# Performance work log

Measured on AMD Instinct MI355X. Metric: run time of the kernel, lower is better.

The kernel has to match this reference:

```python
import jax, jax.numpy as jnp
import numpy as np


def setup_inputs() -> dict:
    key = jax.random.key(0)
    k1, k2, k3 = jax.random.split(key, 3)
    N, C, V, T, K = 32, 64, 25, 1024, 3
    x = jax.random.normal(k1, (N, C, V, T), dtype=jnp.float32)
    # grouped 1x1 conv weight: per node v, maps C -> K*C. torch weight (C*K*V, C, 1, 1)
    W = jax.random.normal(k2, (V, K * C, C), dtype=jnp.float32) * 0.05
    # adjacency buffer A[k, w, v] (src node w -> dst node v, partition k)
    A = jax.random.uniform(k3, (K, V, V), dtype=jnp.float32)
    return {"x": x, "W": W, "A": A}


def reference(x, W, A):
    # x: [N, C, V, T]; W: [V, K*C, C]; A: [K, V, V]
    N, C, V, T = x.shape
    K = A.shape[0]
    # permute(0,2,1,3): [N, V, C, T]; grouped 1x1 conv == per-node matmul C -> K*C
    y = jnp.einsum('ncvt,voc->nvot', x, W)          # [N, V, K*C, T]
    # view (N, V, C*K, T) with output-channel layout o = c*K + k -> split to (C, K)
    y = y.reshape(N, V, C, K, T)                     # [N, V(src=w), C, K, T]
    # einsum('kwv,nckwt->ncvt')
    out = jnp.einsum('kwv,nwckt->ncvt', A, y)        # [N, C, V, T]
    return out
```

## Files before the change

kernel.cpp:

```cpp
#include <hip/hip_runtime.h>

#define Nn 32
#define Cc 64
#define Vv 25
#define Tt 1024

typedef __attribute__((ext_vector_type(4))) float f32x4;
typedef __attribute__((ext_vector_type(8))) short bf16x8;
typedef __attribute__((ext_vector_type(4))) unsigned short u16x4;

__device__ __forceinline__ unsigned short f2bf(float f) {
    union { float f; unsigned u; } a; a.f = f;
    unsigned u = a.u;
    u += 0x7fff + ((u >> 16) & 1);
    return (unsigned short)(u >> 16);
}

__device__ __forceinline__ void gl_lds16(const unsigned short* g, unsigned short* l) {
    __builtin_amdgcn_global_load_lds(
        (const __attribute__((address_space(1))) unsigned int*)g,
        (__attribute__((address_space(3))) unsigned int*)l, 16, 0, 0);
}


__global__ __launch_bounds__(256) void prep_fused(
        const float* __restrict__ x, const float* __restrict__ W,
        const float* __restrict__ A, unsigned short* __restrict__ xb,
        unsigned short* __restrict__ Weff) {
    int bid = blockIdx.x;
    if (bid < Vv * Vv) {
        int v = bid / Vv;
        int w = bid - v * Vv;
        float a0 = A[(0 * Vv + w) * Vv + v];
        float a1 = A[(1 * Vv + w) * Vv + v];
        float a2 = A[(2 * Vv + w) * Vv + v];
        const float* Wb = W + (size_t)w * 192 * 64;
        unsigned short* o = Weff + (size_t)(v * Vv + w) * 4096;
        int c  = threadIdx.x >> 2;
        int c0 = (threadIdx.x & 3) * 16;
        #pragma unroll
        for (int i = 0; i < 16; ++i) {
            int cp = c0 + i;
            float val = a0 * Wb[(c * 3 + 0) * 64 + cp]
                      + a1 * Wb[(c * 3 + 1) * 64 + cp]
                      + a2 * Wb[(c * 3 + 2) * 64 + cp];
            int jl = cp >> 3;
            o[c * 64 + ((jl ^ (c & 7)) << 3) + (cp & 7)] = f2bf(val);
        }
        return;
    }
    int pid = bid - Vv * Vv;
    int n = pid / (Vv * 4);
    int rem = pid - n * (Vv * 4);
    int w = rem >> 2;
    int sl = rem & 3;

    int tid = threadIdx.x;
    int wq = tid >> 6;
    int l  = tid & 63;
    int quad = l >> 4, m = l & 15;

    const float* xw = x + ((size_t)n * Cc * Vv + w) * Tt + sl * 256 + wq * 64 + m;
    unsigned short* dst = xb +
        ((((size_t)(n * Vv + w) * 4 + sl) * 2048) + (size_t)wq * 512 + l) * 8;

    #pragma unroll
    for (int kc = 0; kc < 2; ++kc) {
        float vals[4][8];
        #pragma unroll
        for (int kk = 0; kk < 8; ++kk) {
            int cp = (kc * 4 + quad) * 8 + kk;
            const float* row = xw + (size_t)cp * (Vv * Tt);
            #pragma unroll
            for (int ni = 0; ni < 4; ++ni)
                vals[ni][kk] = __builtin_nontemporal_load(row + ni * 16);
        }
        #pragma unroll
        for (int ni = 0; ni < 4; ++ni) {
            bf16x8 o;
            #pragma unroll
            for (int kk = 0; kk < 8; ++kk) o[kk] = (short)f2bf(vals[ni][kk]);
            *(bf16x8*)&dst[(size_t)(kc * 256 + ni * 64) * 8] = o;
        }
    }
}

__global__ __launch_bounds__(256, 2) void gc_fast(
        const unsigned short* __restrict__ xb,
        const unsigned short* __restrict__ Weff,
        float* __restrict__ out) {
    __shared__ __align__(16) unsigned short wa[4][4096];

    int bid = blockIdx.x;
    int xcd = bid & 7;
    int lid = bid >> 3;
    int v = lid % Vv;
    int s = lid / Vv;
    int slice = (xcd << 4) + s;
    int n  = slice >> 2;
    int sl = slice & 3;
    int t0 = sl << 8;

    int tid = threadIdx.x;
    int lane = tid & 63, wv = tid >> 6;
    int m = lane & 15, quad = lane >> 4;

    const unsigned short* wg = Weff + (size_t)v * (Vv * 4096);
    const unsigned short* xbase = xb + ((size_t)(n * Vv * 4 + sl)) * 2048 * 8;

    int coff0 = ((quad)     ^ (m & 7)) << 3;
    int coff1 = ((4 + quad) ^ (m & 7)) << 3;
    int arow[4];
    #pragma unroll
    for (int mi = 0; mi < 4; ++mi) arow[mi] = (mi * 16 + m) * 64;
    int boff[8];
    #pragma unroll
    for (int q = 0; q < 8; ++q) boff[q] = ((wv * 8 + q) * 64 + lane) * 8;

    f32x4 acc[4][4];
    #pragma unroll
    for (int i = 0; i < 4; ++i)
        #pragma unroll
        for (int j = 0; j < 4; ++j)
            acc[i][j] = (f32x4){0.f, 0.f, 0.f, 0.f};

    bf16x8 b0v[8], b1v[8], b2v[8];
    bf16x8 afA[8], afB[8];

#define SB __builtin_amdgcn_sched_barrier(0)
#define VMCNT(N_) asm volatile("s_waitcnt vmcnt(" #N_ ")" ::: "memory")

#define ISSUE_A(WBUF, w_) do { \
    const unsigned short* s_ = wg + (size_t)(w_) * 4096 + tid * 8; \
    gl_lds16(s_,        &wa[WBUF][tid * 8]); \
    gl_lds16(s_ + 2048, &wa[WBUF][2048 + tid * 8]); \
} while (0)

#define ISSUE_B(BN, w_) do { \
    const unsigned short* xw_ = xbase + (size_t)(w_) * 65536; \
    _Pragma("unroll") \
    for (int q_ = 0; q_ < 8; ++q_) \
        BN[q_] = *(const bf16x8*)(xw_ + boff[q_]); \
} while (0)

#define LDREAD(AF, RBUF) do { \
    const unsigned short* cur_ = &wa[RBUF][0]; \
    _Pragma("unroll") \
    for (int mi_ = 0; mi_ < 4; ++mi_) { \
        AF[mi_]     = *(const bf16x8*)(cur_ + arow[mi_] + coff0); \
        AF[mi_ + 4] = *(const bf16x8*)(cur_ + arow[mi_] + coff1); \
    } \
} while (0)

#define COMP(AF, BC) do { \
    __builtin_amdgcn_s_setprio(1); \
    _Pragma("unroll") \
    for (int mi_ = 0; mi_ < 4; ++mi_) \
        _Pragma("unroll") \
        for (int ni_ = 0; ni_ < 4; ++ni_) \
            acc[mi_][ni_] = __builtin_amdgcn_mfma_f32_16x16x32_bf16( \
                AF[mi_], BC[ni_], acc[mi_][ni_], 0, 0, 0); \
    _Pragma("unroll") \
    for (int mi_ = 0; mi_ < 4; ++mi_) \
        _Pragma("unroll") \
        for (int ni_ = 0; ni_ < 4; ++ni_) \
            acc[mi_][ni_] = __builtin_amdgcn_mfma_f32_16x16x32_bf16( \
                AF[mi_ + 4], BC[ni_ + 4], acc[mi_][ni_], 0, 0, 0); \
    __builtin_amdgcn_s_setprio(0); \
} while (0)

#define STEP(AFc, AFn, WB, RB, BC, BN, w_) do { \
    ISSUE_A(WB, (w_) + 2); \
    ISSUE_B(BN, (w_) + 2); \
    SB; VMCNT(18); SB; \
    __builtin_amdgcn_s_barrier(); \
    SB; \
    COMP(AFc, BC); \
    LDREAD(AFn, RB); \
    SB; \
} while (0)

    ISSUE_A(0, 0);
    ISSUE_A(1, 1);
    ISSUE_B(b0v, 0);
    ISSUE_B(b1v, 1);
    SB; VMCNT(16); SB;
    __builtin_amdgcn_s_barrier();
    SB;
    LDREAD(afA, 0);
    SB;

    STEP(afA, afB, 2, 1, b0v, b2v,  0);
    STEP(afB, afA, 3, 2, b1v, b0v,  1);
    STEP(afA, afB, 0, 3, b2v, b1v,  2);
    STEP(afB, afA, 1, 0, b0v, b2v,  3);
    STEP(afA, afB, 2, 1, b1v, b0v,  4);
    STEP(afB, afA, 3, 2, b2v, b1v,  5);
    STEP(afA, afB, 0, 3, b0v, b2v,  6);
    STEP(afB, afA, 1, 0, b1v, b0v,  7);
    STEP(afA, afB, 2, 1, b2v, b1v,  8);
    STEP(afB, afA, 3, 2, b0v, b2v,  9);
    STEP(afA, afB, 0, 3, b1v, b0v, 10);
    STEP(afB, afA, 1, 0, b2v, b1v, 11);
    STEP(afA, afB, 2, 1, b0v, b2v, 12);
    STEP(afB, afA, 3, 2, b1v, b0v, 13);
    STEP(afA, afB, 0, 3, b2v, b1v, 14);
    STEP(afB, afA, 1, 0, b0v, b2v, 15);
    STEP(afA, afB, 2, 1, b1v, b0v, 16);
    STEP(afB, afA, 3, 2, b2v, b1v, 17);
    STEP(afA, afB, 0, 3, b0v, b2v, 18);
    STEP(afB, afA, 1, 0, b1v, b0v, 19);
    STEP(afA, afB, 2, 1, b2v, b1v, 20);
    STEP(afB, afA, 3, 2, b0v, b2v, 21);
    STEP(afA, afB, 0, 3, b1v, b0v, 22);
    SB; VMCNT(8); SB;
    __builtin_amdgcn_s_barrier();
    SB;
    COMP(afB, b2v);
    LDREAD(afA, 0);
    SB;
    VMCNT(0);
    SB;
    COMP(afA, b0v);

#undef STEP
#undef COMP
#undef LDREAD
#undef ISSUE_B
#undef ISSUE_A
#undef VMCNT
#undef SB

    float* og = out + ((size_t)n * Cc * Vv + v) * Tt + t0 + wv * 64 + m;
    #pragma unroll
    for (int mi = 0; mi < 4; ++mi)
        #pragma unroll
        for (int r = 0; r < 4; ++r) {
            int c = mi * 16 + quad * 4 + r;
            float* orow = og + (size_t)c * Vv * Tt;
            #pragma unroll
            for (int ni = 0; ni < 4; ++ni)
                __builtin_nontemporal_store(acc[mi][ni][r], &orow[ni * 16]);
        }
}


__global__ __launch_bounds__(256) void weff_prep_plain(
        const float* __restrict__ W, const float* __restrict__ A,
        unsigned short* __restrict__ Weff) {
    int v = blockIdx.x / Vv;
    int w = blockIdx.x - v * Vv;
    float a0 = A[(0 * Vv + w) * Vv + v];
    float a1 = A[(1 * Vv + w) * Vv + v];
    float a2 = A[(2 * Vv + w) * Vv + v];
    const float* Wb = W + (size_t)w * 192 * 64;
    unsigned short* o = Weff + (size_t)(v * Vv + w) * 4096;
    int e0 = threadIdx.x * 16;
    #pragma unroll
    for (int i = 0; i < 16; ++i) {
        int e = e0 + i;
        int c = e >> 6, cp = e & 63;
        float val = a0 * Wb[(c * 3 + 0) * 64 + cp]
                  + a1 * Wb[(c * 3 + 1) * 64 + cp]
                  + a2 * Wb[(c * 3 + 2) * 64 + cp];
        o[e] = f2bf(val);
    }
}

__global__ __launch_bounds__(256, 2) void gc_plain(
        const float* __restrict__ x, const unsigned short* __restrict__ Weff,
        float* __restrict__ out) {
    __shared__ __align__(16) unsigned short xs[256 * 72];
    __shared__ __align__(16) unsigned short wa[64 * 72];
    int bid = blockIdx.x;
    int xcd = bid & 7;
    int lid = bid >> 3;
    int v, s;
    if (lid < 13 * 16) { v = lid % 13;            s = lid / 13; }
    else { int l2 = lid - 13 * 16; v = 13 + l2 % 12; s = l2 / 12; }
    int slice = (xcd << 4) + s;
    int n  = slice >> 2;
    int t0 = (slice & 3) << 8;
    int tid  = threadIdx.x;
    int lane = tid & 63;
    int wv   = tid >> 6;
    int m    = lane & 15;
    int quad = lane >> 4;
    int cc = tid & 7;
    int tt = tid >> 3;
    f32x4 acc[4][4];
    #pragma unroll
    for (int i = 0; i < 4; ++i)
        #pragma unroll
        for (int j = 0; j < 4; ++j)
            acc[i][j] = (f32x4){0.f, 0.f, 0.f, 0.f};
    const float* xg = x + (size_t)n * Cc * Vv * Tt + t0 + tt * 4;
    const bf16x8* wg = (const bf16x8*)(Weff + (size_t)v * Vv * 4096);
    for (int w = 0; w < Vv; ++w) {
        if (w) __syncthreads();
        #pragma unroll
        for (int r = 0; r < 2; ++r) {
            int q = r * 256 + tid;
            int c = q >> 3, b = q & 7;
            *(bf16x8*)&wa[c * 72 + b * 8] = wg[w * 512 + q];
        }
        {
            bf16x8 rows[8];
            #pragma unroll
            for (int i = 0; i < 8; ++i) {
                int cp = cc * 8 + i;
                const float* p = xg + ((size_t)cp * Vv + w) * Tt;
                float4 f0 = *(const float4*)p;
                float4 f1 = *(const float4*)(p + 128);
                rows[0][i] = (short)f2bf(f0.x); rows[1][i] = (short)f2bf(f0.y);
                rows[2][i] = (short)f2bf(f0.z); rows[3][i] = (short)f2bf(f0.w);
                rows[4][i] = (short)f2bf(f1.x); rows[5][i] = (short)f2bf(f1.y);
                rows[6][i] = (short)f2bf(f1.z); rows[7][i] = (short)f2bf(f1.w);
            }
            #pragma unroll
            for (int j = 0; j < 4; ++j) {
                *(bf16x8*)&xs[(tt * 4 + j) * 72 + cc * 8]       = rows[j];
                *(bf16x8*)&xs[(128 + tt * 4 + j) * 72 + cc * 8] = rows[4 + j];
            }
        }
        __syncthreads();
        #pragma unroll
        for (int kc = 0; kc < 2; ++kc) {
            int ko = kc * 32 + quad * 8;
            bf16x8 afr[4], bfr[4];
            #pragma unroll
            for (int mi = 0; mi < 4; ++mi)
                afr[mi] = *(const bf16x8*)&wa[(mi * 16 + m) * 72 + ko];
            #pragma unroll
            for (int ni = 0; ni < 4; ++ni)
                bfr[ni] = *(const bf16x8*)&xs[(wv * 64 + ni * 16 + m) * 72 + ko];
            #pragma unroll
            for (int mi = 0; mi < 4; ++mi)
                #pragma unroll
                for (int ni = 0; ni < 4; ++ni)
                    acc[mi][ni] = __builtin_amdgcn_mfma_f32_16x16x32_bf16(
                        afr[mi], bfr[ni], acc[mi][ni], 0, 0, 0);
        }
    }
    float* og = out + ((size_t)n * Cc * Vv + v) * Tt + t0 + wv * 64 + m;
    #pragma unroll
    for (int mi = 0; mi < 4; ++mi)
        #pragma unroll
        for (int r = 0; r < 4; ++r) {
            int c = mi * 16 + quad * 4 + r;
            float* orow = og + (size_t)c * Vv * Tt;
            #pragma unroll
            for (int ni = 0; ni < 4; ++ni)
                orow[ni * 16] = acc[mi][ni][r];
        }
}

extern "C" void kernel_launch(void* const* d_in, const int* in_sizes, int n_in,
                              void* d_out, int out_size, void* d_ws, size_t ws_size,
                              hipStream_t stream) {
    const float* x = (const float*)d_in[0];
    const float* W = (const float*)d_in[1];
    const float* A = (const float*)d_in[2];
    float* out = (float*)d_out;

    const size_t xb_elems   = (size_t)Nn * Vv * Tt * 64;
    const size_t weff_elems = (size_t)Vv * Vv * 4096;
    const size_t need = (xb_elems + weff_elems) * sizeof(unsigned short);

    if (ws_size >= need) {
        unsigned short* xb   = (unsigned short*)d_ws;
        unsigned short* Weff = xb + xb_elems;
        prep_fused<<<dim3(Vv * Vv + Nn * Vv * 4), dim3(256), 0, stream>>>(x, W, A, xb, Weff);
        gc_fast<<<dim3(3200), dim3(256), 0, stream>>>(xb, Weff, out);
    } else {
        unsigned short* Weff = (unsigned short*)d_ws;
        weff_prep_plain<<<dim3(Vv * Vv), dim3(256), 0, stream>>>(W, A, Weff);
        gc_plain<<<dim3(3200), dim3(256), 0, stream>>>(x, Weff, out);
    }
}
```

Baseline: 492.3 us.

## Load effective weights directly into registers in MFMA fragment layout, drop LDS staging

The prep kernel now writes Weff pre-arranged in the per-lane MFMA A-fragment order, replacing the XOR-swizzled row layout. The main kernel then loads A fragments straight from global memory into registers, removing the LDS buffers, the global-to-LDS async copies, the LDS reads and the per-step workgroup barriers. The cost is that every wave fetches the full weight tile from global/L2 on its own instead of sharing one LDS copy per block, and the pipeline has more outstanding vector loads per step.

```diff
diff --git a/kernel.cpp b/kernel.cpp
--- a/kernel.cpp
+++ b/kernel.cpp
@@ -14,12 +14,6 @@
     unsigned u = a.u;
     u += 0x7fff + ((u >> 16) & 1);
     return (unsigned short)(u >> 16);
-}
-
-__device__ __forceinline__ void gl_lds16(const unsigned short* g, unsigned short* l) {
-    __builtin_amdgcn_global_load_lds(
-        (const __attribute__((address_space(1))) unsigned int*)g,
-        (__attribute__((address_space(3))) unsigned int*)l, 16, 0, 0);
 }
 
 
@@ -36,16 +30,24 @@
         float a2 = A[(2 * Vv + w) * Vv + v];
         const float* Wb = W + (size_t)w * 192 * 64;
         unsigned short* o = Weff + (size_t)(v * Vv + w) * 4096;
-        int c  = threadIdx.x >> 2;
-        int c0 = (threadIdx.x & 3) * 16;
-        #pragma unroll
-        for (int i = 0; i < 16; ++i) {
-            int cp = c0 + i;
-            float val = a0 * Wb[(c * 3 + 0) * 64 + cp]
-                      + a1 * Wb[(c * 3 + 1) * 64 + cp]
-                      + a2 * Wb[(c * 3 + 2) * 64 + cp];
-            int jl = cp >> 3;
-            o[c * 64 + ((jl ^ (c & 7)) << 3) + (cp & 7)] = f2bf(val);
+        int tid = threadIdx.x;
+        int mi = tid >> 6;
+        int lane = tid & 63;
+        int m = lane & 15, quad = lane >> 4;
+        int c = mi * 16 + m;
+        const float* r0 = Wb + (size_t)(c * 3 + 0) * 64;
+        const float* r1 = Wb + (size_t)(c * 3 + 1) * 64;
+        const float* r2 = Wb + (size_t)(c * 3 + 2) * 64;
+        #pragma unroll
+        for (int kc = 0; kc < 2; ++kc) {
+            bf16x8 ov;
+            #pragma unroll
+            for (int kk = 0; kk < 8; ++kk) {
+                int cp = kc * 32 + quad * 8 + kk;
+                float val = a0 * r0[cp] + a1 * r1[cp] + a2 * r2[cp];
+                ov[kk] = (short)f2bf(val);
+            }
+            *(bf16x8*)&o[((kc * 4 + mi) * 64 + lane) * 8] = ov;
         }
         return;
     }
@@ -89,8 +91,6 @@
         const unsigned short* __restrict__ xb,
         const unsigned short* __restrict__ Weff,
         float* __restrict__ out) {
-    __shared__ __align__(16) unsigned short wa[4][4096];
-
     int bid = blockIdx.x;
     int xcd = bid & 7;
     int lid = bid >> 3;
@@ -105,14 +105,9 @@
     int lane = tid & 63, wv = tid >> 6;
     int m = lane & 15, quad = lane >> 4;
 
-    const unsigned short* wg = Weff + (size_t)v * (Vv * 4096);
+    const unsigned short* wg = Weff + (size_t)v * (Vv * 4096) + (size_t)lane * 8;
     const unsigned short* xbase = xb + ((size_t)(n * Vv * 4 + sl)) * 2048 * 8;
 
-    int coff0 = ((quad)     ^ (m & 7)) << 3;
-    int coff1 = ((4 + quad) ^ (m & 7)) << 3;
-    int arow[4];
-    #pragma unroll
-    for (int mi = 0; mi < 4; ++mi) arow[mi] = (mi * 16 + m) * 64;
     int boff[8];
     #pragma unroll
     for (int q = 0; q < 8; ++q) boff[q] = ((wv * 8 + q) * 64 + lane) * 8;
@@ -130,10 +125,11 @@
 #define SB __builtin_amdgcn_sched_barrier(0)
 #define VMCNT(N_) asm volatile("s_waitcnt vmcnt(" #N_ ")" ::: "memory")
 
-#define ISSUE_A(WBUF, w_) do { \
-    const unsigned short* s_ = wg + (size_t)(w_) * 4096 + tid * 8; \
-    gl_lds16(s_,        &wa[WBUF][tid * 8]); \
-    gl_lds16(s_ + 2048, &wa[WBUF][2048 + tid * 8]); \
+#define ISSUE_AF(AF, w_) do { \
+    const unsigned short* aw_ = wg + (size_t)(w_) * 4096; \
+    _Pragma("unroll") \
+    for (int j_ = 0; j_ < 8; ++j_) \
+        AF[j_] = *(const bf16x8*)(aw_ + (size_t)j_ * 512); \
 } while (0)
 
 #define ISSUE_B(BN, w_) do { \
@@ -141,15 +137,6 @@
     _Pragma("unroll") \
     for (int q_ = 0; q_ < 8; ++q_) \
         BN[q_] = *(const bf16x8*)(xw_ + boff[q_]); \
-} while (0)
-
-#define LDREAD(AF, RBUF) do { \
-    const unsigned short* cur_ = &wa[RBUF][0]; \
-    _Pragma("unroll") \
-    for (int mi_ = 0; mi_ < 4; ++mi_) { \
-        AF[mi_]     = *(const bf16x8*)(cur_ + arow[mi_] + coff0); \
-        AF[mi_ + 4] = *(const bf16x8*)(cur_ + arow[mi_] + coff1); \
-    } \
 } while (0)
 
 #define COMP(AF, BC) do { \
@@ -169,55 +156,45 @@
     __builtin_amdgcn_s_setprio(0); \
 } while (0)
 
-#define STEP(AFc, AFn, WB, RB, BC, BN, w_) do { \
-    ISSUE_A(WB, (w_) + 2); \
+#define STEP(AFc, AFn, BC, BN, w_) do { \
+    ISSUE_AF(AFn, (w_) + 1); \
     ISSUE_B(BN, (w_) + 2); \
-    SB; VMCNT(18); SB; \
-    __builtin_amdgcn_s_barrier(); \
-    SB; \
+    SB; VMCNT(24); SB; \
     COMP(AFc, BC); \
-    LDREAD(AFn, RB); \
     SB; \
 } while (0)
 
-    ISSUE_A(0, 0);
-    ISSUE_A(1, 1);
     ISSUE_B(b0v, 0);
+    ISSUE_AF(afA, 0);
     ISSUE_B(b1v, 1);
+    SB;
+
+    STEP(afA, afB, b0v, b2v,  0);
+    STEP(afB, afA, b1v, b0v,  1);
+    STEP(afA, afB, b2v, b1v,  2);
+    STEP(afB, afA, b0v, b2v,  3);
+    STEP(afA, afB, b1v, b0v,  4);
+    STEP(afB, afA, b2v, b1v,  5);
+    STEP(afA, afB, b0v, b2v,  6);
+    STEP(afB, afA, b1v, b0v,  7);
+    STEP(afA, afB, b2v, b1v,  8);
+    STEP(afB, afA, b0v, b2v,  9);
+    STEP(afA, afB, b1v, b0v, 10);
+    STEP(afB, afA, b2v, b1v, 11);
+    STEP(afA, afB, b0v, b2v, 12);
+    STEP(afB, afA, b1v, b0v, 13);
+    STEP(afA, afB, b2v, b1v, 14);
+    STEP(afB, afA, b0v, b2v, 15);
+    STEP(afA, afB, b1v, b0v, 16);
+    STEP(afB, afA, b2v, b1v, 17);
+    STEP(afA, afB, b0v, b2v, 18);
+    STEP(afB, afA, b1v, b0v, 19);
+    STEP(afA, afB, b2v, b1v, 20);
+    STEP(afB, afA, b0v, b2v, 21);
+    STEP(afA, afB, b1v, b0v, 22);
+    ISSUE_AF(afA, 24);
     SB; VMCNT(16); SB;
-    __builtin_amdgcn_s_barrier();
-    SB;
-    LDREAD(afA, 0);
-    SB;
-
-    STEP(afA, afB, 2, 1, b0v, b2v,  0);
-    STEP(afB, afA, 3, 2, b1v, b0v,  1);
-    STEP(afA, afB, 0, 3, b2v, b1v,  2);
-    STEP(afB, afA, 1, 0, b0v, b2v,  3);
-    STEP(afA, afB, 2, 1, b1v, b0v,  4);
-    STEP(afB, afA, 3, 2, b2v, b1v,  5);
-    STEP(afA, afB, 0, 3, b0v, b2v,  6);
-    STEP(afB, afA, 1, 0, b1v, b0v,  7);
-    STEP(afA, afB, 2, 1, b2v, b1v,  8);
-    STEP(afB, afA, 3, 2, b0v, b2v,  9);
-    STEP(afA, afB, 0, 3, b1v, b0v, 10);
-    STEP(afB, afA, 1, 0, b2v, b1v, 11);
-    STEP(afA, afB, 2, 1, b0v, b2v, 12);
-    STEP(afB, afA, 3, 2, b1v, b0v, 13);
-    STEP(afA, afB, 0, 3, b2v, b1v, 14);
-    STEP(afB, afA, 1, 0, b0v, b2v, 15);
-    STEP(afA, afB, 2, 1, b1v, b0v, 16);
-    STEP(afB, afA, 3, 2, b2v, b1v, 17);
-    STEP(afA, afB, 0, 3, b0v, b2v, 18);
-    STEP(afB, afA, 1, 0, b1v, b0v, 19);
-    STEP(afA, afB, 2, 1, b2v, b1v, 20);
-    STEP(afB, afA, 3, 2, b0v, b2v, 21);
-    STEP(afA, afB, 0, 3, b1v, b0v, 22);
-    SB; VMCNT(8); SB;
-    __builtin_amdgcn_s_barrier();
-    SB;
     COMP(afB, b2v);
-    LDREAD(afA, 0);
     SB;
     VMCNT(0);
     SB;
@@ -225,9 +202,8 @@
 
 #undef STEP
 #undef COMP
-#undef LDREAD
 #undef ISSUE_B
-#undef ISSUE_A
+#undef ISSUE_AF
 #undef VMCNT
 #undef SB
 
```

After: 517.7 us. 5.2% more time.
